# Kernel optimization log

Measured on AMD Instinct MI355X. Metric: run time of the kernel, lower is better.

Reference implementation:

```python
import jax, jax.numpy as jnp
import numpy as np

EMBED_DIM = 1024
NUM_HEADS = 16
HEAD_DIM = EMBED_DIM // NUM_HEADS
SCALING = HEAD_DIM ** -0.5


def setup_inputs() -> dict:
    key = jax.random.key(0)
    ks = jax.random.split(key, 10)
    B, T, D = 4, 2048, EMBED_DIM
    s = 0.02
    return {
        "hidden_states": jax.random.normal(ks[0], (B, T, D), jnp.float32),
        "attention_mask": jnp.zeros((B, 1, T, T), jnp.float32),
        "Wq": jax.random.normal(ks[1], (D, D), jnp.float32) * s,
        "bq": jnp.zeros((D,), jnp.float32),
        "Wk": jax.random.normal(ks[2], (D, D), jnp.float32) * s,
        "bk": jnp.zeros((D,), jnp.float32),
        "Wv": jax.random.normal(ks[3], (D, D), jnp.float32) * s,
        "bv": jnp.zeros((D,), jnp.float32),
        "Wo": jax.random.normal(ks[4], (D, D), jnp.float32) * s,
        "bo": jnp.zeros((D,), jnp.float32),
    }


def reference(hidden_states, attention_mask, Wq, bq, Wk, bk, Wv, bv, Wo, bo):
    B, T, D = hidden_states.shape
    H, Hd = NUM_HEADS, HEAD_DIM
    # projections (torch Linear: x @ W.T + b; here W stored as (D_in, D_out))
    q = (hidden_states @ Wq + bq) * SCALING
    k = hidden_states @ Wk + bk
    v = hidden_states @ Wv + bv
    q = q.reshape(B, T, H, Hd).transpose(0, 2, 1, 3)  # [B,H,T,Hd]
    k = k.reshape(B, T, H, Hd).transpose(0, 2, 1, 3)
    v = v.reshape(B, T, H, Hd).transpose(0, 2, 1, 3)
    # eager attention: full [B,H,T,T] scores + additive mask + softmax
    scores = jnp.einsum("bhtd,bhsd->bhts", q, k)
    scores = scores + attention_mask[:, :, :, : k.shape[2]]
    attn_weights = jax.nn.softmax(scores, axis=-1)
    attn_output = jnp.einsum("bhts,bhsd->bhtd", attn_weights, v)
    attn_output = attn_output.transpose(0, 2, 1, 3).reshape(B, T, D)
    attn_output = attn_output @ Wo + bo
    return attn_output
```

## Files before the change

kernel.cpp:

```cpp
#include <hip/hip_runtime.h>
#include <hip/hip_bf16.h>
#include <cstdint>

#define TT 2048
#define DD 1024
#define NH 16
#define HD 64
#define NB 4
#define SCALING 0.125f
#define LOG2E 1.44269504088896340736f
#define QSCALE (0.125f * 1.44269504088896340736f)

typedef __bf16 bf16;
typedef __attribute__((ext_vector_type(8))) __bf16 bf16x8;
typedef __attribute__((ext_vector_type(4))) __bf16 bf16x4;
typedef __attribute__((ext_vector_type(4))) float f32x4;

__device__ __forceinline__ void gload_lds16(const bf16* g, bf16* l) {
    __builtin_amdgcn_global_load_lds(
        (__attribute__((address_space(1))) const void*)g,
        (__attribute__((address_space(3))) void*)l, 16, 0, 0);
}

__global__ __launch_bounds__(256) void k_prep(const float* __restrict__ x, bf16* __restrict__ xb,
                                              const float* __restrict__ Wq, const float* __restrict__ Wk,
                                              const float* __restrict__ Wv, const float* __restrict__ Wo,
                                              bf16* __restrict__ Wt) {
    __shared__ float tile_s[32][33];
    int bid = blockIdx.x, tid = threadIdx.x;
    if (bid < 8192) {
        size_t i = ((size_t)bid * 256 + tid) * 4;
        float4 v = *(const float4*)(x + i);
        bf16x4 o;
        o[0] = (bf16)v.x; o[1] = (bf16)v.y; o[2] = (bf16)v.z; o[3] = (bf16)v.w;
        *(bf16x4*)(xb + i) = o;
        return;
    }
    int b2 = bid - 8192;
    int mat = b2 >> 10, tl = b2 & 1023;
    int n0 = (tl & 31) * 32, k0 = (tl >> 5) * 32;
    const float* w = mat == 0 ? Wq : (mat == 1 ? Wk : (mat == 2 ? Wv : Wo));
    int tx = tid & 31, ty = tid >> 5;
#pragma unroll
    for (int i = 0; i < 4; i++)
        tile_s[ty + 8 * i][tx] = w[(size_t)(k0 + ty + 8 * i) * DD + n0 + tx];
    __syncthreads();
#pragma unroll
    for (int i = 0; i < 4; i++)
        Wt[(size_t)mat * DD * DD + (size_t)(n0 + ty + 8 * i) * DD + k0 + tx] = (bf16)tile_s[tx][ty + 8 * i];
}

__device__ __forceinline__ void gemm128_main(const bf16* __restrict__ A, const bf16* __restrict__ Bt,
                                             int m0, int n0, int K,
                                             bf16* smem, f32x4 acc[4][4]) {
    const int tid = threadIdx.x;
    const int w = tid >> 6, lane = tid & 63;
    const int wr = w >> 1, wc = w & 1, quad = lane >> 4, l16 = lane & 15;
    f32x4 zero = {0.f, 0.f, 0.f, 0.f};
#pragma unroll
    for (int mi = 0; mi < 4; mi++)
#pragma unroll
        for (int ni = 0; ni < 4; ni++) acc[mi][ni] = zero;

    int cidx[4], goff[4];
#pragma unroll
    for (int j = 0; j < 4; j++) {
        int idx = (w * 4 + j) * 64 + lane;
        int row = idx >> 3, m = idx & 7;
        cidx[j] = idx * 8;
        goff[j] = row * K + (m ^ (row & 7)) * 8;
    }
    const bf16* Ab = A + (size_t)m0 * K;
    const bf16* Bb = Bt + (size_t)n0 * K;

    for (int k0 = 0; k0 < K; k0 += 64) {
        if (k0) __syncthreads();
#pragma unroll
        for (int j = 0; j < 4; j++) {
            gload_lds16(Ab + k0 + goff[j], smem + cidx[j]);
            gload_lds16(Bb + k0 + goff[j], smem + 8192 + cidx[j]);
        }
        __syncthreads();
#pragma unroll
        for (int kd = 0; kd < 2; kd++) {
            const int csw = ((kd * 4 + quad) ^ (l16 & 7)) * 8;
            bf16x8 af[4], bfv[4];
#pragma unroll
            for (int i = 0; i < 4; i++)
                af[i] = *(const bf16x8*)(smem + (wr * 64 + i * 16 + l16) * 64 + csw);
#pragma unroll
            for (int i = 0; i < 4; i++)
                bfv[i] = *(const bf16x8*)(smem + 8192 + (wc * 64 + i * 16 + l16) * 64 + csw);
#pragma unroll
            for (int mi = 0; mi < 4; mi++)
#pragma unroll
                for (int ni = 0; ni < 4; ni++)
                    acc[mi][ni] = __builtin_amdgcn_mfma_f32_16x16x32_bf16(af[mi], bfv[ni], acc[mi][ni], 0, 0, 0);
        }
    }
}

__global__ __launch_bounds__(256) void k_gemm_qkv(const bf16* __restrict__ Xb, const bf16* __restrict__ Wt,
                                                  const float* __restrict__ bq, const float* __restrict__ bk,
                                                  const float* __restrict__ bv,
                                                  bf16* __restrict__ qb, bf16* __restrict__ kb,
                                                  bf16* __restrict__ vt,
                                                  const float* __restrict__ mask, int* __restrict__ flags) {
    __shared__ bf16 smem[16384];
    __shared__ int s_any[4];
    const int bid = blockIdx.x, tid = threadIdx.x;
    const int grp = bid / 7, rem = bid % 7;

    if (rem >= 3) {
        int fid = grp * 4 + (rem - 3);
        int st = fid & 31, tt = (fid >> 5) & 15, bbm = fid >> 9;
        const float* mp = mask + ((size_t)bbm * TT + tt * 128) * TT + st * 64;
        int c = (tid & 15) * 4;
        int r0 = tid >> 4;
        int any = 0;
        for (int r = r0; r < 128; r += 16) {
            float4 v = *(const float4*)(mp + (size_t)r * TT + c);
            any |= (v.x != 0.f) | (v.y != 0.f) | (v.z != 0.f) | (v.w != 0.f);
        }
        any = __any(any) ? 1 : 0;
        if ((tid & 63) == 0) s_any[tid >> 6] = any;
        __syncthreads();
        if (tid == 0)
            flags[(bbm * 16 + tt) * 32 + st] = s_any[0] | s_any[1] | s_any[2] | s_any[3];
        return;
    }

    int g = grp * 3 + rem;
    int bx = g % 24, by = g / 24;
    int m0 = by * 128, n0 = bx * 128;
    f32x4 acc[4][4];
    gemm128_main(Xb, Wt, m0, n0, DD, smem, acc);

    const int w = tid >> 6, lane = tid & 63;
    const int wr = w >> 1, wc = w & 1, quad = lane >> 4, l16 = lane & 15;
    const int which = n0 >> 10;
    const int bbk = m0 >> 11, tbase = m0 & 2047;
    const int nn0 = n0 & 1023;

    if (which < 2) {
        const float* bias = which == 0 ? bq : bk;
        bf16* dst = which == 0 ? qb : kb;
        const float scl = which == 0 ? QSCALE : 1.0f;
#pragma unroll
        for (int phase = 0; phase < 2; phase++) {
            __syncthreads();
            if (wc == phase) {
#pragma unroll
                for (int mi = 0; mi < 4; mi++)
#pragma unroll
                    for (int ni = 0; ni < 4; ni++) {
                        int d = ni * 16 + l16;
                        float bb_ = bias[nn0 + phase * 64 + d];
#pragma unroll
                        for (int r = 0; r < 4; r++) {
                            int t_l = wr * 64 + mi * 16 + quad * 4 + r;
                            smem[t_l * 72 + d] = (bf16)((acc[mi][ni][r] + bb_) * scl);
                        }
                    }
            }
            __syncthreads();
            int hh = (nn0 + phase * 64) >> 6;
            bf16* dp = dst + (((size_t)bbk * NH + hh) * TT + tbase) * HD;
#pragma unroll
            for (int i = 0; i < 4; i++) {
                int idx = i * 256 + tid;
                int rr = idx >> 3, cc = (idx & 7) * 8;
                *(bf16x8*)(dp + (size_t)rr * HD + cc) = *(const bf16x8*)(smem + rr * 72 + cc);
            }
        }
    } else {
#pragma unroll
        for (int phase = 0; phase < 2; phase++) {
            __syncthreads();
            if (wc == phase) {
#pragma unroll
                for (int mi = 0; mi < 4; mi++)
#pragma unroll
                    for (int ni = 0; ni < 4; ni++) {
                        int nn_l = ni * 16 + l16;
                        float bb_ = bv[nn0 + phase * 64 + nn_l];
#pragma unroll
                        for (int r = 0; r < 4; r++)
                            smem[nn_l * 132 + wr * 64 + quad * 16 + mi * 4 + r] = (bf16)(acc[mi][ni][r] + bb_);
                    }
            }
            __syncthreads();
            int hh = (nn0 + phase * 64) >> 6;
#pragma unroll
            for (int i = 0; i < 4; i++) {
                int idx = i * 256 + tid;
                int rr = idx >> 4, cc = (idx & 15) * 8;
                bf16x8 vv = *(const bf16x8*)(smem + rr * 132 + cc);
                *(bf16x8*)(vt + (((size_t)bbk * NH + hh) * HD + rr) * TT + tbase + cc) = vv;
            }
        }
    }
}

__global__ __launch_bounds__(256, 4) void k_attn(const bf16* __restrict__ qb, const bf16* __restrict__ kb,
                                                 const bf16* __restrict__ vt, const float* __restrict__ mask,
                                                 const int* __restrict__ flags, bf16* __restrict__ ob) {
    __shared__ bf16 SB[4][4096];
    __shared__ int s_anyflag;

    const int tq0 = blockIdx.x * 128;
    const int h = blockIdx.y, bb = blockIdx.z;
    const int tid = threadIdx.x, w = tid >> 6, lane = tid & 63;
    const int quad = lane >> 4, l16 = lane & 15;

    const bf16* Qg = qb + (((size_t)bb * NH + h) * TT + tq0) * HD;
    const bf16* Kg = kb + ((size_t)bb * NH + h) * TT * HD;
    const bf16* Vg = vt + ((size_t)bb * NH + h) * HD * TT;

    int cidx[2], koff[2], voff[2];
#pragma unroll
    for (int j = 0; j < 2; j++) {
        int idx = (w * 2 + j) * 64 + lane;
        int row = idx >> 3, m = idx & 7;
        cidx[j] = idx * 8;
        koff[j] = row * HD + ((m ^ (row & 7)) * 8);
        voff[j] = row * TT + ((m ^ (row & 7)) * 8);
    }

#pragma unroll
    for (int j = 0; j < 4; j++) {
        int idx = (w * 4 + j) * 64 + lane;
        int row = idx >> 3, m = idx & 7;
        gload_lds16(Qg + row * HD + (m ^ (row & 7)) * 8, &SB[2][0] + idx * 8);
    }
#pragma unroll
    for (int j = 0; j < 2; j++) {
        gload_lds16(Kg + koff[j], SB[0] + cidx[j]);
        gload_lds16(Vg + voff[j], SB[1] + cidx[j]);
    }

    const int fbase = (bb * 16 + blockIdx.x) * 32;
    {
        int f0 = (tid < 32) ? flags[fbase + tid] : 0;
        if (tid < 64) { int a = __any(f0 != 0) ? 1 : 0; if (tid == 0) s_anyflag = a; }
    }

    bf16x8 ones;
#pragma unroll
    for (int i = 0; i < 8; i++) ones[i] = (bf16)1.0f;

    f32x4 oa[2][4];
    f32x4 lacc[2];
    f32x4 zero = {0.f, 0.f, 0.f, 0.f};
#pragma unroll
    for (int qi = 0; qi < 2; qi++) {
        lacc[qi] = zero;
#pragma unroll
        for (int ni = 0; ni < 4; ni++) oa[qi][ni] = zero;
    }

    __syncthreads();
    const int anyflag = s_anyflag;

    bf16x8 aq[2][2];
#pragma unroll
    for (int kd = 0; kd < 2; kd++) {
        const int csw = ((kd * 4 + quad) ^ (l16 & 7)) * 8;
#pragma unroll
        for (int qi = 0; qi < 2; qi++)
            aq[kd][qi] = *(const bf16x8*)(&SB[2][0] + (w * 32 + qi * 16 + l16) * 64 + csw);
    }

#define ATTN_COMPUTE(Ks, Vs, S0)                                                              \
    {                                                                                         \
        f32x4 st[4][2];                                                                       \
        _Pragma("unroll") for (int si = 0; si < 4; si++)                                      \
            _Pragma("unroll") for (int qi = 0; qi < 2; qi++) st[si][qi] = zero;               \
        _Pragma("unroll") for (int kd = 0; kd < 2; kd++) {                                    \
            const int csw = ((kd * 4 + quad) ^ (l16 & 7)) * 8;                                \
            bf16x8 kf[4];                                                                     \
            _Pragma("unroll") for (int si = 0; si < 4; si++)                                  \
                kf[si] = *(const bf16x8*)((Ks) + (si * 16 + l16) * 64 + csw);                 \
            _Pragma("unroll") for (int si = 0; si < 4; si++)                                  \
                _Pragma("unroll") for (int qi = 0; qi < 2; qi++)                              \
                    st[si][qi] = __builtin_amdgcn_mfma_f32_16x16x32_bf16(kf[si], aq[kd][qi],  \
                                                                        st[si][qi], 0, 0, 0);\
        }                                                                                     \
        if (anyflag && flags[fbase + ((S0) >> 6)]) {                                          \
            const float* mp = mask + ((size_t)bb * TT + tq0) * TT + (S0);                     \
            _Pragma("unroll") for (int si = 0; si < 4; si++)                                  \
                _Pragma("unroll") for (int qi = 0; qi < 2; qi++)                              \
                    _Pragma("unroll") for (int r = 0; r < 4; r++)                             \
                        st[si][qi][r] += mp[(size_t)(w * 32 + qi * 16 + l16) * TT             \
                                            + si * 16 + quad * 4 + r] * LOG2E;                \
        }                                                                                     \
        bf16 ep[4][2][4];                                                                     \
        _Pragma("unroll") for (int si = 0; si < 4; si++)                                      \
            _Pragma("unroll") for (int qi = 0; qi < 2; qi++)                                  \
                _Pragma("unroll") for (int r = 0; r < 4; r++)                                 \
                    ep[si][qi][r] = (bf16)exp2f(st[si][qi][r]);                               \
        _Pragma("unroll") for (int kk = 0; kk < 2; kk++) {                                    \
            bf16x8 ap[2];                                                                     \
            _Pragma("unroll") for (int qi = 0; qi < 2; qi++)                                  \
                _Pragma("unroll") for (int j = 0; j < 8; j++)                                 \
                    ap[qi][j] = ep[2 * kk + (j >> 2)][qi][j & 3];                             \
            bf16x8 bv8[4];                                                                    \
            _Pragma("unroll") for (int ni = 0; ni < 4; ni++)                                  \
                bv8[ni] = *(const bf16x8*)((Vs) + (ni * 16 + l16) * 64                        \
                                           + ((quad * 2 + kk) ^ (l16 & 7)) * 8);              \
            _Pragma("unroll") for (int qi = 0; qi < 2; qi++)                                  \
                lacc[qi] = __builtin_amdgcn_mfma_f32_16x16x32_bf16(ap[qi], ones, lacc[qi],    \
                                                                   0, 0, 0);                  \
            _Pragma("unroll") for (int qi = 0; qi < 2; qi++)                                  \
                _Pragma("unroll") for (int ni = 0; ni < 4; ni++)                              \
                    oa[qi][ni] = __builtin_amdgcn_mfma_f32_16x16x32_bf16(ap[qi], bv8[ni],     \
                                                                         oa[qi][ni], 0, 0, 0);\
        }                                                                                     \
    }

    ATTN_COMPUTE(SB[0], SB[1], 0)
    __syncthreads();
#pragma unroll
    for (int j = 0; j < 2; j++) {
        gload_lds16(Kg + 64 * HD + koff[j], SB[2] + cidx[j]);
        gload_lds16(Vg + 64 + voff[j], SB[3] + cidx[j]);
    }
    __syncthreads();

    for (int i = 1; i < 32; i++) {
        const int cur = i & 1, nxt = cur ^ 1;
        if (i < 31) {
            const int sn = (i + 1) * 64;
#pragma unroll
            for (int j = 0; j < 2; j++) {
                gload_lds16(Kg + sn * HD + koff[j], SB[2 * nxt] + cidx[j]);
                gload_lds16(Vg + sn + voff[j], SB[2 * nxt + 1] + cidx[j]);
            }
        }
        ATTN_COMPUTE(SB[2 * cur], SB[2 * cur + 1], i * 64)
        __syncthreads();
    }
#undef ATTN_COMPUTE

#pragma unroll
    for (int qi = 0; qi < 2; qi++)
#pragma unroll
        for (int r = 0; r < 4; r++) {
            float inv = 1.f / lacc[qi][r];
            int trow = tq0 + w * 32 + qi * 16 + quad * 4 + r;
#pragma unroll
            for (int ni = 0; ni < 4; ni++) {
                float v = oa[qi][ni][r] * inv;
                ob[((size_t)bb * TT + trow) * DD + h * HD + ni * 16 + l16] = (bf16)v;
            }
        }
}

__global__ __launch_bounds__(256) void k_gemm_out(const bf16* __restrict__ Ob, const bf16* __restrict__ Wot,
                                                  const float* __restrict__ bo, float* __restrict__ out) {
    __shared__ bf16 smem[16384];
    int m0 = blockIdx.y * 128, n0 = blockIdx.x * 128;
    f32x4 acc[4][4];
    gemm128_main(Ob, Wot, m0, n0, DD, smem, acc);

    const int tid = threadIdx.x, w = tid >> 6, lane = tid & 63;
    const int wr = w >> 1, wc = w & 1, quad = lane >> 4, l16 = lane & 15;
#pragma unroll
    for (int mi = 0; mi < 4; mi++)
#pragma unroll
        for (int ni = 0; ni < 4; ni++) {
            int gn = n0 + wc * 64 + ni * 16 + l16;
            float bb_ = bo[gn];
#pragma unroll
            for (int r = 0; r < 4; r++) {
                int gm = m0 + wr * 64 + mi * 16 + quad * 4 + r;
                out[(size_t)gm * DD + gn] = acc[mi][ni][r] + bb_;
            }
        }
}

extern "C" void kernel_launch(void* const* d_in, const int* in_sizes, int n_in,
                              void* d_out, int out_size, void* d_ws, size_t ws_size,
                              hipStream_t stream) {
    const float* hidden = (const float*)d_in[0];
    const float* mask   = (const float*)d_in[1];
    const float* Wq     = (const float*)d_in[2];
    const float* bq     = (const float*)d_in[3];
    const float* Wk     = (const float*)d_in[4];
    const float* bk     = (const float*)d_in[5];
    const float* Wv     = (const float*)d_in[6];
    const float* bv     = (const float*)d_in[7];
    const float* Wo     = (const float*)d_in[8];
    const float* bo     = (const float*)d_in[9];
    float* out = (float*)d_out;
    char* ws = (char*)d_ws;

    const size_t MB = 1024 * 1024;
    bf16* Xb   = (bf16*)(ws);
    bf16* Wt   = (bf16*)(ws + 16 * MB);
    bf16* qb   = (bf16*)(ws + 24 * MB);
    bf16* kb   = (bf16*)(ws + 40 * MB);
    bf16* vt   = (bf16*)(ws + 56 * MB);
    bf16* ob   = (bf16*)(ws + 72 * MB);
    int* flags = (int*)(ws + 88 * MB);

    hipLaunchKernelGGL(k_prep, dim3(12288), dim3(256), 0, stream, hidden, Xb, Wq, Wk, Wv, Wo, Wt);
    hipLaunchKernelGGL(k_gemm_qkv, dim3(3584), dim3(256), 0, stream, Xb, Wt, bq, bk, bv, qb, kb, vt, mask, flags);
    hipLaunchKernelGGL(k_attn, dim3(16, 16, 4), dim3(256), 0, stream, qb, kb, vt, mask, flags, ob);
    hipLaunchKernelGGL(k_gemm_out, dim3(8, 64), dim3(256), 0, stream, ob, Wt + (size_t)3 * DD * DD, bo, out);
}
```

Before: 360.7 us.

## Double KV tile to 128 keys, remap blocks by XCD, issue prefetch earlier

The attention kernel now loads 128 keys per stage instead of 64, halving the number of loop iterations and barriers. The first prefetch is issued before the first compute, and a barrier is added after the Q fragments are read into registers. The grid becomes 1D and is remapped so the query tiles of one batch-head land on the same XCD, aiming for better L2 reuse of K and V. LDS use doubles and launch bounds drop to 2 blocks per CU, which may cut occupancy. Compute is split into four 32-key sub-chunks to limit register pressure.

```diff
diff --git a/kernel.cpp b/kernel.cpp
--- a/kernel.cpp
+++ b/kernel.cpp
@@ -202,14 +202,18 @@
     }
 }
 
-__global__ __launch_bounds__(256, 4) void k_attn(const bf16* __restrict__ qb, const bf16* __restrict__ kb,
+__global__ __launch_bounds__(256, 2) void k_attn(const bf16* __restrict__ qb, const bf16* __restrict__ kb,
                                                  const bf16* __restrict__ vt, const float* __restrict__ mask,
                                                  const int* __restrict__ flags, bf16* __restrict__ ob) {
-    __shared__ bf16 SB[4][4096];
+    __shared__ bf16 SB[4][8192];
     __shared__ int s_anyflag;
 
-    const int tq0 = blockIdx.x * 128;
-    const int h = blockIdx.y, bb = blockIdx.z;
+    const int id = blockIdx.x;
+    const int xcd = id & 7, jj = id >> 3;
+    const int qt = jj & 15, bh = ((jj >> 4) << 3) | xcd;
+    const int h = bh & 15, bb = bh >> 4;
+    const int tq0 = qt * 128;
+
     const int tid = threadIdx.x, w = tid >> 6, lane = tid & 63;
     const int quad = lane >> 4, l16 = lane & 15;
 
@@ -217,14 +221,15 @@
     const bf16* Kg = kb + ((size_t)bb * NH + h) * TT * HD;
     const bf16* Vg = vt + ((size_t)bb * NH + h) * HD * TT;
 
-    int cidx[2], koff[2], voff[2];
-#pragma unroll
-    for (int j = 0; j < 2; j++) {
-        int idx = (w * 2 + j) * 64 + lane;
-        int row = idx >> 3, m = idx & 7;
+    int cidx[4], koff[4], voff[4];
+#pragma unroll
+    for (int j = 0; j < 4; j++) {
+        int idx = (w * 4 + j) * 64 + lane;
         cidx[j] = idx * 8;
-        koff[j] = row * HD + ((m ^ (row & 7)) * 8);
-        voff[j] = row * TT + ((m ^ (row & 7)) * 8);
+        int krow = idx >> 3, km = idx & 7;
+        koff[j] = krow * HD + (km ^ (krow & 7)) * 8;
+        int d = idx >> 4, c = idx & 15;
+        voff[j] = d * TT + ((c & 8) + ((c & 7) ^ (d & 7))) * 8;
     }
 
 #pragma unroll
@@ -234,12 +239,12 @@
         gload_lds16(Qg + row * HD + (m ^ (row & 7)) * 8, &SB[2][0] + idx * 8);
     }
 #pragma unroll
-    for (int j = 0; j < 2; j++) {
+    for (int j = 0; j < 4; j++) {
         gload_lds16(Kg + koff[j], SB[0] + cidx[j]);
         gload_lds16(Vg + voff[j], SB[1] + cidx[j]);
     }
 
-    const int fbase = (bb * 16 + blockIdx.x) * 32;
+    const int fbase = (bb * 16 + qt) * 32;
     {
         int f0 = (tid < 32) ? flags[fbase + tid] : 0;
         if (tid < 64) { int a = __any(f0 != 0) ? 1 : 0; if (tid == 0) s_anyflag = a; }
@@ -270,44 +275,45 @@
         for (int qi = 0; qi < 2; qi++)
             aq[kd][qi] = *(const bf16x8*)(&SB[2][0] + (w * 32 + qi * 16 + l16) * 64 + csw);
     }
+    __syncthreads();
 
 #define ATTN_COMPUTE(Ks, Vs, S0)                                                              \
     {                                                                                         \
-        f32x4 st[4][2];                                                                       \
-        _Pragma("unroll") for (int si = 0; si < 4; si++)                                      \
-            _Pragma("unroll") for (int qi = 0; qi < 2; qi++) st[si][qi] = zero;               \
-        _Pragma("unroll") for (int kd = 0; kd < 2; kd++) {                                    \
-            const int csw = ((kd * 4 + quad) ^ (l16 & 7)) * 8;                                \
-            bf16x8 kf[4];                                                                     \
-            _Pragma("unroll") for (int si = 0; si < 4; si++)                                  \
-                kf[si] = *(const bf16x8*)((Ks) + (si * 16 + l16) * 64 + csw);                 \
-            _Pragma("unroll") for (int si = 0; si < 4; si++)                                  \
-                _Pragma("unroll") for (int qi = 0; qi < 2; qi++)                              \
-                    st[si][qi] = __builtin_amdgcn_mfma_f32_16x16x32_bf16(kf[si], aq[kd][qi],  \
-                                                                        st[si][qi], 0, 0, 0);\
-        }                                                                                     \
-        if (anyflag && flags[fbase + ((S0) >> 6)]) {                                          \
-            const float* mp = mask + ((size_t)bb * TT + tq0) * TT + (S0);                     \
-            _Pragma("unroll") for (int si = 0; si < 4; si++)                                  \
+        _Pragma("unroll") for (int pp = 0; pp < 4; pp++) {                                    \
+            f32x4 st2[2][2];                                                                  \
+            _Pragma("unroll") for (int si = 0; si < 2; si++)                                  \
+                _Pragma("unroll") for (int qi = 0; qi < 2; qi++) st2[si][qi] = zero;          \
+            _Pragma("unroll") for (int kd = 0; kd < 2; kd++) {                                \
+                const int csw = ((kd * 4 + quad) ^ (l16 & 7)) * 8;                            \
+                bf16x8 kf[2];                                                                 \
+                _Pragma("unroll") for (int si = 0; si < 2; si++)                              \
+                    kf[si] = *(const bf16x8*)((Ks) + ((pp * 2 + si) * 16 + l16) * 64 + csw);  \
+                _Pragma("unroll") for (int si = 0; si < 2; si++)                              \
+                    _Pragma("unroll") for (int qi = 0; qi < 2; qi++)                          \
+                        st2[si][qi] = __builtin_amdgcn_mfma_f32_16x16x32_bf16(                \
+                            kf[si], aq[kd][qi], st2[si][qi], 0, 0, 0);                        \
+            }                                                                                 \
+            if (anyflag && flags[fbase + ((S0) >> 6) + (pp >> 1)]) {                          \
+                const float* mp = mask + ((size_t)bb * TT + tq0) * TT + (S0) + pp * 32;       \
+                _Pragma("unroll") for (int si = 0; si < 2; si++)                              \
+                    _Pragma("unroll") for (int qi = 0; qi < 2; qi++)                          \
+                        _Pragma("unroll") for (int r = 0; r < 4; r++)                         \
+                            st2[si][qi][r] += mp[(size_t)(w * 32 + qi * 16 + l16) * TT        \
+                                                 + si * 16 + quad * 4 + r] * LOG2E;           \
+            }                                                                                 \
+            bf16 ep[2][2][4];                                                                 \
+            _Pragma("unroll") for (int si = 0; si < 2; si++)                                  \
                 _Pragma("unroll") for (int qi = 0; qi < 2; qi++)                              \
                     _Pragma("unroll") for (int r = 0; r < 4; r++)                             \
-                        st[si][qi][r] += mp[(size_t)(w * 32 + qi * 16 + l16) * TT             \
-                                            + si * 16 + quad * 4 + r] * LOG2E;                \
-        }                                                                                     \
-        bf16 ep[4][2][4];                                                                     \
-        _Pragma("unroll") for (int si = 0; si < 4; si++)                                      \
-            _Pragma("unroll") for (int qi = 0; qi < 2; qi++)                                  \
-                _Pragma("unroll") for (int r = 0; r < 4; r++)                                 \
-                    ep[si][qi][r] = (bf16)exp2f(st[si][qi][r]);                               \
-        _Pragma("unroll") for (int kk = 0; kk < 2; kk++) {                                    \
+                        ep[si][qi][r] = (bf16)exp2f(st2[si][qi][r]);                          \
             bf16x8 ap[2];                                                                     \
             _Pragma("unroll") for (int qi = 0; qi < 2; qi++)                                  \
                 _Pragma("unroll") for (int j = 0; j < 8; j++)                                 \
-                    ap[qi][j] = ep[2 * kk + (j >> 2)][qi][j & 3];                             \
+                    ap[qi][j] = ep[j >> 2][qi][j & 3];                                        \
             bf16x8 bv8[4];                                                                    \
             _Pragma("unroll") for (int ni = 0; ni < 4; ni++)                                  \
-                bv8[ni] = *(const bf16x8*)((Vs) + (ni * 16 + l16) * 64                        \
-                                           + ((quad * 2 + kk) ^ (l16 & 7)) * 8);              \
+                bv8[ni] = *(const bf16x8*)((Vs) + (ni * 16 + l16) * 128                       \
+                    + ((pp >> 1) * 8 + ((quad * 2 + (pp & 1)) ^ (l16 & 7))) * 8);             \
             _Pragma("unroll") for (int qi = 0; qi < 2; qi++)                                  \
                 lacc[qi] = __builtin_amdgcn_mfma_f32_16x16x32_bf16(ap[qi], ones, lacc[qi],    \
                                                                    0, 0, 0);                  \
@@ -318,26 +324,25 @@
         }                                                                                     \
     }
 
+#pragma unroll
+    for (int j = 0; j < 4; j++) {
+        gload_lds16(Kg + 128 * HD + koff[j], SB[2] + cidx[j]);
+        gload_lds16(Vg + 128 + voff[j], SB[3] + cidx[j]);
+    }
     ATTN_COMPUTE(SB[0], SB[1], 0)
     __syncthreads();
-#pragma unroll
-    for (int j = 0; j < 2; j++) {
-        gload_lds16(Kg + 64 * HD + koff[j], SB[2] + cidx[j]);
-        gload_lds16(Vg + 64 + voff[j], SB[3] + cidx[j]);
-    }
-    __syncthreads();
-
-    for (int i = 1; i < 32; i++) {
+
+    for (int i = 1; i < 16; i++) {
         const int cur = i & 1, nxt = cur ^ 1;
-        if (i < 31) {
-            const int sn = (i + 1) * 64;
-#pragma unroll
-            for (int j = 0; j < 2; j++) {
+        if (i < 15) {
+            const int sn = (i + 1) * 128;
+#pragma unroll
+            for (int j = 0; j < 4; j++) {
                 gload_lds16(Kg + sn * HD + koff[j], SB[2 * nxt] + cidx[j]);
                 gload_lds16(Vg + sn + voff[j], SB[2 * nxt + 1] + cidx[j]);
             }
         }
-        ATTN_COMPUTE(SB[2 * cur], SB[2 * cur + 1], i * 64)
+        ATTN_COMPUTE(SB[2 * cur], SB[2 * cur + 1], i * 128)
         __syncthreads();
     }
 #undef ATTN_COMPUTE
@@ -406,6 +411,6 @@
 
     hipLaunchKernelGGL(k_prep, dim3(12288), dim3(256), 0, stream, hidden, Xb, Wq, Wk, Wv, Wo, Wt);
     hipLaunchKernelGGL(k_gemm_qkv, dim3(3584), dim3(256), 0, stream, Xb, Wt, bq, bk, bv, qb, kb, vt, mask, flags);
-    hipLaunchKernelGGL(k_attn, dim3(16, 16, 4), dim3(256), 0, stream, qb, kb, vt, mask, flags, ob);
+    hipLaunchKernelGGL(k_attn, dim3(1024), dim3(256), 0, stream, qb, kb, vt, mask, flags, ob);
     hipLaunchKernelGGL(k_gemm_out, dim3(8, 64), dim3(256), 0, stream, ob, Wt + (size_t)3 * DD * DD, bo, out);
 }
```

Measured after the change: 362.0 us. About the same (+0.4%).
